# Kernel tuning notes

Hardware: AMD Instinct MI355X
Metric: run time of the kernel (lower is better)

Reference implementation:

```python
import jax, jax.numpy as jnp
import numpy as np

B, WK, HRS = 2048, 52, 8760
DT = 0.125          # Euler step in days (3-hourly), exactly representable
RANGE_PRED = 7      # forecast horizon in days


def setup_inputs() -> dict:
    key = jax.random.key(0)
    k1, k2, k3, k4 = jax.random.split(key, 4)
    # X_in: [B, weeks, 5, 1]; channel 0 = start time in days (same across batch,
    # the torch code reads X_in[0, week, 0, 0]); channels 1..4 = N,P,Z,D init.
    X_in = jax.random.uniform(k1, (B, WK, 5, 1), jnp.float32, 0.1, 3.0)
    t0 = jnp.arange(WK, dtype=jnp.float32) * 7.0
    X_in = X_in.at[:, :, 0, 0].set(jnp.broadcast_to(t0, (B, WK)))
    global_f = jax.random.uniform(k2, (B, HRS), jnp.float32)          # light forcing in [0,1]
    global_m = jax.random.uniform(k3, (B, HRS), jnp.float32) * 0.1    # mixing rate, small
    params_value = jax.random.uniform(k4, (B, 10), jnp.float32, 0.1, 1.0)
    return {"X_in": X_in, "global_f": global_f, "global_m": global_m,
            "params_value": params_value, "dt": DT, "range_pred": RANGE_PRED}


def reference(X_in, global_f, global_m, params_value, dt, range_pred):
    # Fixed multipliers from the torch code
    pv = jnp.asarray([1.0, 2.0, 0.1, 0.05, 0.1, 0.3, 0.6, 0.15, 0.4, 0.1], X_in.dtype)
    Q0, Vm, thr = 8.0, 1.0, 0.01  # Q0 = 4 + 2.5 + 1.5 + 0
    chi, rho, gam, lam, eps, alp, bet, eta, phi, zet = [params_value[:, i][:, None] for i in range(10)]  # [B,1]

    n_steps = int(round(range_pred / dt))      # 56
    stride = int(round(1.0 / dt))              # 8 -> daily sampling of output

    # Hourly forcing gather: same time axis for every batch element (torch uses X_in[0,...])
    t0 = X_in[0, :, 0, 0]                                                     # [W]
    times = t0[:, None] + jnp.arange(n_steps + 1, dtype=X_in.dtype) * dt      # [W, S]
    idx = jnp.round(times * 24.0).astype(jnp.int32)
    f = jnp.take(global_f, idx, axis=1)[:, :, :n_steps]                       # [B, W, T]
    m = jnp.take(global_m, idx, axis=1)[:, :, :n_steps]

    def step(carry, ft_mt):
        N, P, Z, D = carry                      # each [B, W]
        ft, mt = ft_mt
        Pc = jnp.maximum(thr, P)
        Zc = jnp.maximum(thr, Z)
        gN = N / (chi * pv[0] + N)
        zg = rho * pv[1] * (1.0 - jnp.exp(-lam * pv[3] * Pc)) * Zc
        up = Vm * gN * ft * Pc
        Nn = N + dt * (-up + alp * pv[5] * zg + eps * pv[4] * P + gam * pv[2] * Z + phi * pv[8] * D + mt * (Q0 - N))
        Pn = P + dt * (up - zg - eps * pv[4] * P - eta * pv[7] * P - mt * P)
        Zn = Z + dt * (bet * pv[6] * zg - gam * pv[2] * Z - mt * Z)
        Dn = D + dt * (eta * pv[7] * P + (1.0 - alp * pv[5] - bet * pv[6]) * zg - phi * pv[8] * D - zet * pv[9] * D - mt * D)
        new = (Nn, Pn, Zn, Dn)
        return new, jnp.stack(new, axis=0)      # [4, B, W]

    carry0 = (X_in[:, :, 1, 0], X_in[:, :, 2, 0], X_in[:, :, 3, 0], X_in[:, :, 4, 0])
    _, ys = jax.lax.scan(step, carry0, (jnp.moveaxis(f, 2, 0), jnp.moveaxis(m, 2, 0)))  # ys: [T, 4, B, W]
    traj = jnp.concatenate([jnp.stack(carry0, axis=0)[None], ys], axis=0)               # [S, 4, B, W]
    out = jnp.moveaxis(traj, (0, 1), (3, 2))                                            # [B, W, 4, S]
    return out[:, :, :, ::stride]               # daily samples: [B, W, 4, range_pred+1]
```

## Files before the change

kernel.cpp:

```cpp
#include <hip/hip_runtime.h>


typedef float f32x4 __attribute__((ext_vector_type(4)));

#define NPZD_B 2048
#define NPZD_WK 52
#define NPZD_HRS 8760
#define NPZD_WKH 26
#define NPZD_CS 28
#define NPZD_F4C 21
#define NPZD_NI 546
#define NPZD_LDSW (NPZD_WKH * NPZD_CS)

__global__ __launch_bounds__(64, 4) void npzd_kernel(
    const float* __restrict__ X_in,
    const float* __restrict__ gf,
    const float* __restrict__ gm,
    const float* __restrict__ params,
    const float* __restrict__ dt_ptr,
    float* __restrict__ out)
{
    __shared__ __align__(16) float lds_f[NPZD_LDSW];
    __shared__ __align__(16) float lds_m[NPZD_LDSW];

    const int bid  = blockIdx.x;
    const int b    = bid >> 1;
    const int hb   = bid & 1;
    const int lane = threadIdx.x;

    const float dt = dt_ptr[0];
    const int wl = (lane < NPZD_WKH) ? lane : (NPZD_WKH - 1);
    const int wg = NPZD_WKH * hb + wl;
    const float* xb = X_in + ((size_t)b * NPZD_WK + wg) * 5;
    const float x1 = xb[1], x2 = xb[2], x3 = xb[3], x4 = xb[4];

    const float* pp = params + (size_t)b * 10;
    const float chi   = pp[0];
    const float rho2  = pp[1] * 2.0f;
    const float gam1  = pp[2] * 0.1f;
    const float lam05 = pp[3] * 0.05f;
    const float eps1  = pp[4] * 0.1f;
    const float alp3  = pp[5] * 0.3f;
    const float bet6  = pp[6] * 0.6f;
    const float eta15 = pp[7] * 0.15f;
    const float phi4  = pp[8] * 0.4f;
    const float zet1  = pp[9] * 0.1f;
    const float rem   = 1.0f - alp3 - bet6;

    const f32x4* __restrict__ gf4 = (const f32x4*)(gf + (size_t)b * NPZD_HRS);
    const f32x4* __restrict__ gm4 = (const f32x4*)(gm + (size_t)b * NPZD_HRS);

    float N = x1, P = x2, Z = x3, D = x4;
    float oN[8], oP[8], oZ[8], oD[8];
    oN[0] = N; oP[0] = P; oZ[0] = Z; oD[0] = D;

    #pragma unroll
    for (int c = 0; c < 2; ++c) {
        f32x4 fv[9], mv[9];
        int ii[9];
        #pragma unroll
        for (int t = 0; t < 9; ++t) {
            int i = t * 64 + lane;
            if (i >= NPZD_NI) i = NPZD_NI - 1;
            ii[t] = i;
            const int w = (i * 49933) >> 20;
            const int f = i - 21 * w;
            const int k = 42 * (NPZD_WKH * hb + w) + NPZD_F4C * c + f;
            fv[t] = gf4[k];
            mv[t] = gm4[k];
        }

        if (c) __syncthreads();

        #pragma unroll
        for (int t = 0; t < 9; ++t) {
            const int i = ii[t];
            const int w = (i * 49933) >> 20;
            const int f = i - 21 * w;
            const float fe[4] = {fv[t].x, fv[t].y, fv[t].z, fv[t].w};
            const float me[4] = {mv[t].x, mv[t].y, mv[t].z, mv[t].w};
            const int rm = f % 3;
            const int e0 = (rm == 0) ? 0 : (3 - rm);
            const int tp = (4 * f + e0) / 3;
            const int p  = NPZD_CS * w + tp;
            lds_f[p] = fe[e0];
            lds_m[p] = me[e0];
            if (rm == 0) {
                lds_f[p + 1] = fe[3];
                lds_m[p + 1] = me[3];
            }
        }
        __syncthreads();

        if (lane < NPZD_WKH) {
            const float* lf = lds_f + wl * NPZD_CS;
            const float* lm = lds_m + wl * NPZD_CS;
            #pragma unroll
            for (int g = 0; g < 7; ++g) {
                const f32x4 f4 = *(const f32x4*)(lf + 4 * g);
                const f32x4 m4 = *(const f32x4*)(lm + 4 * g);
                const float fs[4] = {f4.x, f4.y, f4.z, f4.w};
                const float ms[4] = {m4.x, m4.y, m4.z, m4.w};
                #pragma unroll
                for (int q = 0; q < 4; ++q) {
                    const float ft = fs[q], mt = ms[q];
                    const float Pc = fmaxf(0.01f, P);
                    const float Zc = fmaxf(0.01f, Z);
                    const float gN = N * __builtin_amdgcn_rcpf(chi + N);
                    const float zg = rho2 * (1.0f - __expf(-lam05 * Pc)) * Zc;
                    const float up = gN * ft * Pc;
                    const float Nn = N + dt * (-up + alp3 * zg + eps1 * P + gam1 * Z + phi4 * D + mt * (8.0f - N));
                    const float Pn = P + dt * (up - zg - eps1 * P - eta15 * P - mt * P);
                    const float Zn = Z + dt * (bet6 * zg - gam1 * Z - mt * Z);
                    const float Dn = D + dt * (eta15 * P + rem * zg - phi4 * D - zet1 * D - mt * D);
                    N = Nn; P = Pn; Z = Zn; D = Dn;
                }
                const int g14 = 7 * c + g;
                if (g14 & 1) {
                    const int co = (g14 >> 1) + 1;
                    oN[co] = N; oP[co] = P; oZ[co] = Z; oD[co] = D;
                }
            }
        }
    }

    if (lane >= NPZD_WKH) return;
    f32x4* o4 = (f32x4*)(out + ((size_t)b * NPZD_WK + wg) * 32);
    o4[0] = (f32x4){oN[0], oN[1], oN[2], oN[3]};
    o4[1] = (f32x4){oN[4], oN[5], oN[6], oN[7]};
    o4[2] = (f32x4){oP[0], oP[1], oP[2], oP[3]};
    o4[3] = (f32x4){oP[4], oP[5], oP[6], oP[7]};
    o4[4] = (f32x4){oZ[0], oZ[1], oZ[2], oZ[3]};
    o4[5] = (f32x4){oZ[4], oZ[5], oZ[6], oZ[7]};
    o4[6] = (f32x4){oD[0], oD[1], oD[2], oD[3]};
    o4[7] = (f32x4){oD[4], oD[5], oD[6], oD[7]};
}

extern "C" void kernel_launch(void* const* d_in, const int* in_sizes, int n_in,
                              void* d_out, int out_size, void* d_ws, size_t ws_size,
                              hipStream_t stream) {
    const float* X_in   = (const float*)d_in[0];
    const float* gf     = (const float*)d_in[1];
    const float* gm     = (const float*)d_in[2];
    const float* params = (const float*)d_in[3];
    const float* dt_ptr = (const float*)d_in[4];
    float* out = (float*)d_out;

    npzd_kernel<<<NPZD_B * 2, 64, 0, stream>>>(X_in, gf, gm, params, dt_ptr, out);
}
```

Baseline: 189.5 us.

## Double-buffer per-day forcing loads directly into LDS with async global_load_lds

Replaces the two-chunk load, register-shuffle and LDS-scatter scheme with seven per-day chunks fetched by global_load_lds straight into a double-buffered LDS area. The next day's forcing is loaded while the current day is integrated, with manual vmcnt waits in place of __syncthreads. Stride-3 LDS reads pick the hourly samples, so the compaction scatter and extra barriers go away. It relies on single-wave blocks and hand-counted waitcnts for correctness, and reads LDS at stride 3 instead of with vector loads.

```diff
diff --git a/kernel.cpp b/kernel.cpp
--- a/kernel.cpp
+++ b/kernel.cpp
@@ -7,10 +7,22 @@
 #define NPZD_WK 52
 #define NPZD_HRS 8760
 #define NPZD_WKH 26
-#define NPZD_CS 28
-#define NPZD_F4C 21
-#define NPZD_NI 546
-#define NPZD_LDSW (NPZD_WKH * NPZD_CS)
+#define NPZD_CS 8
+#define NPZD_F4C 6
+#define NPZD_NI 156
+#define NPZD_SLOTS 192
+
+typedef const __attribute__((address_space(1))) void* gas_t;
+typedef __attribute__((address_space(3))) void* las_t;
+
+#define NPZD_ISSUE(c, d) do { \
+    __builtin_amdgcn_global_load_lds((gas_t)(const void*)(gf4 + kb0 + 6*(c)), (las_t)(void*)&lds[d][0][0],   16, 0, 0); \
+    __builtin_amdgcn_global_load_lds((gas_t)(const void*)(gf4 + kb1 + 6*(c)), (las_t)(void*)&lds[d][0][64],  16, 0, 0); \
+    __builtin_amdgcn_global_load_lds((gas_t)(const void*)(gf4 + kb2 + 6*(c)), (las_t)(void*)&lds[d][0][128], 16, 0, 0); \
+    __builtin_amdgcn_global_load_lds((gas_t)(const void*)(gm4 + kb0 + 6*(c)), (las_t)(void*)&lds[d][1][0],   16, 0, 0); \
+    __builtin_amdgcn_global_load_lds((gas_t)(const void*)(gm4 + kb1 + 6*(c)), (las_t)(void*)&lds[d][1][64],  16, 0, 0); \
+    __builtin_amdgcn_global_load_lds((gas_t)(const void*)(gm4 + kb2 + 6*(c)), (las_t)(void*)&lds[d][1][128], 16, 0, 0); \
+} while (0)
 
 __global__ __launch_bounds__(64, 4) void npzd_kernel(
     const float* __restrict__ X_in,
@@ -20,19 +32,36 @@
     const float* __restrict__ dt_ptr,
     float* __restrict__ out)
 {
-    __shared__ __align__(16) float lds_f[NPZD_LDSW];
-    __shared__ __align__(16) float lds_m[NPZD_LDSW];
+    __shared__ __align__(16) f32x4 lds[2][2][NPZD_SLOTS];
 
     const int bid  = blockIdx.x;
     const int b    = bid >> 1;
     const int hb   = bid & 1;
     const int lane = threadIdx.x;
 
+    const f32x4* __restrict__ gf4 = (const f32x4*)(gf + (size_t)b * NPZD_HRS);
+    const f32x4* __restrict__ gm4 = (const f32x4*)(gm + (size_t)b * NPZD_HRS);
+
+    int kb0, kb1, kb2;
+    {
+        const int i0 = lane;
+        const int i1 = 64 + lane;
+        int i2 = 128 + lane; if (i2 >= NPZD_NI) i2 = NPZD_NI - 1;
+        const int w0 = (i0 * 43691) >> 18, f0 = i0 - 6 * w0;
+        const int w1 = (i1 * 43691) >> 18, f1 = i1 - 6 * w1;
+        const int w2 = (i2 * 43691) >> 18, f2 = i2 - 6 * w2;
+        kb0 = 1092 * hb + 42 * w0 + f0;
+        kb1 = 1092 * hb + 42 * w1 + f1;
+        kb2 = 1092 * hb + 42 * w2 + f2;
+    }
+
+    NPZD_ISSUE(0, 0);
+
     const float dt = dt_ptr[0];
     const int wl = (lane < NPZD_WKH) ? lane : (NPZD_WKH - 1);
     const int wg = NPZD_WKH * hb + wl;
     const float* xb = X_in + ((size_t)b * NPZD_WK + wg) * 5;
-    const float x1 = xb[1], x2 = xb[2], x3 = xb[3], x4 = xb[4];
+    float N = xb[1], P = xb[2], Z = xb[3], D = xb[4];
 
     const float* pp = params + (size_t)b * 10;
     const float chi   = pp[0];
@@ -47,80 +76,39 @@
     const float zet1  = pp[9] * 0.1f;
     const float rem   = 1.0f - alp3 - bet6;
 
-    const f32x4* __restrict__ gf4 = (const f32x4*)(gf + (size_t)b * NPZD_HRS);
-    const f32x4* __restrict__ gm4 = (const f32x4*)(gm + (size_t)b * NPZD_HRS);
-
-    float N = x1, P = x2, Z = x3, D = x4;
     float oN[8], oP[8], oZ[8], oD[8];
     oN[0] = N; oP[0] = P; oZ[0] = Z; oD[0] = D;
 
     #pragma unroll
-    for (int c = 0; c < 2; ++c) {
-        f32x4 fv[9], mv[9];
-        int ii[9];
-        #pragma unroll
-        for (int t = 0; t < 9; ++t) {
-            int i = t * 64 + lane;
-            if (i >= NPZD_NI) i = NPZD_NI - 1;
-            ii[t] = i;
-            const int w = (i * 49933) >> 20;
-            const int f = i - 21 * w;
-            const int k = 42 * (NPZD_WKH * hb + w) + NPZD_F4C * c + f;
-            fv[t] = gf4[k];
-            mv[t] = gm4[k];
+    for (int c = 0; c < 7; ++c) {
+        const int d = c & 1;
+        if (c < 6) {
+            NPZD_ISSUE(c + 1, d ^ 1);
+            asm volatile("s_waitcnt vmcnt(6)" ::: "memory");
+        } else {
+            asm volatile("s_waitcnt vmcnt(0)" ::: "memory");
         }
-
-        if (c) __syncthreads();
-
-        #pragma unroll
-        for (int t = 0; t < 9; ++t) {
-            const int i = ii[t];
-            const int w = (i * 49933) >> 20;
-            const int f = i - 21 * w;
-            const float fe[4] = {fv[t].x, fv[t].y, fv[t].z, fv[t].w};
-            const float me[4] = {mv[t].x, mv[t].y, mv[t].z, mv[t].w};
-            const int rm = f % 3;
-            const int e0 = (rm == 0) ? 0 : (3 - rm);
-            const int tp = (4 * f + e0) / 3;
-            const int p  = NPZD_CS * w + tp;
-            lds_f[p] = fe[e0];
-            lds_m[p] = me[e0];
-            if (rm == 0) {
-                lds_f[p + 1] = fe[3];
-                lds_m[p + 1] = me[3];
-            }
-        }
-        __syncthreads();
+        __builtin_amdgcn_sched_barrier(0);
 
         if (lane < NPZD_WKH) {
-            const float* lf = lds_f + wl * NPZD_CS;
-            const float* lm = lds_m + wl * NPZD_CS;
+            const float* lf = (const float*)&lds[d][0][0] + 24 * wl;
+            const float* lm = (const float*)&lds[d][1][0] + 24 * wl;
             #pragma unroll
-            for (int g = 0; g < 7; ++g) {
-                const f32x4 f4 = *(const f32x4*)(lf + 4 * g);
-                const f32x4 m4 = *(const f32x4*)(lm + 4 * g);
-                const float fs[4] = {f4.x, f4.y, f4.z, f4.w};
-                const float ms[4] = {m4.x, m4.y, m4.z, m4.w};
-                #pragma unroll
-                for (int q = 0; q < 4; ++q) {
-                    const float ft = fs[q], mt = ms[q];
-                    const float Pc = fmaxf(0.01f, P);
-                    const float Zc = fmaxf(0.01f, Z);
-                    const float gN = N * __builtin_amdgcn_rcpf(chi + N);
-                    const float zg = rho2 * (1.0f - __expf(-lam05 * Pc)) * Zc;
-                    const float up = gN * ft * Pc;
-                    const float Nn = N + dt * (-up + alp3 * zg + eps1 * P + gam1 * Z + phi4 * D + mt * (8.0f - N));
-                    const float Pn = P + dt * (up - zg - eps1 * P - eta15 * P - mt * P);
-                    const float Zn = Z + dt * (bet6 * zg - gam1 * Z - mt * Z);
-                    const float Dn = D + dt * (eta15 * P + rem * zg - phi4 * D - zet1 * D - mt * D);
-                    N = Nn; P = Pn; Z = Zn; D = Dn;
-                }
-                const int g14 = 7 * c + g;
-                if (g14 & 1) {
-                    const int co = (g14 >> 1) + 1;
-                    oN[co] = N; oP[co] = P; oZ[co] = Z; oD[co] = D;
-                }
+            for (int s = 0; s < NPZD_CS; ++s) {
+                const float ft = lf[3 * s];
+                const float mt = lm[3 * s];
+                const float Pc = fmaxf(0.01f, P);
+                const float Zc = fmaxf(0.01f, Z);
+                const float gN = N * __builtin_amdgcn_rcpf(chi + N);
+                const float zg = rho2 * (1.0f - __expf(-lam05 * Pc)) * Zc;
+                const float up = gN * ft * Pc;
+                const float Nn = N + dt * (-up + alp3 * zg + eps1 * P + gam1 * Z + phi4 * D + mt * (8.0f - N));
+                const float Pn = P + dt * (up - zg - eps1 * P - eta15 * P - mt * P);
+                const float Zn = Z + dt * (bet6 * zg - gam1 * Z - mt * Z);
+                const float Dn = D + dt * (eta15 * P + rem * zg - phi4 * D - zet1 * D - mt * D);
+                N = Nn; P = Pn; Z = Zn; D = Dn;
             }
+            oN[c + 1] = N; oP[c + 1] = P; oZ[c + 1] = Z; oD[c + 1] = D;
         }
     }
 
```

Measured after the change: 251.2 us. +32.6%, slower.
